# Optimization experiments

Measured on AMD Instinct MI355X. Metric: run time of the kernel, lower is better.

Reference implementation:

```python
import jax, jax.numpy as jnp
import numpy as np

# RBF_Conv2d config (matches init_kwargs)
KH = KW = 3
STRIDE = 1
OUT_CH = 256
IN_CH = 64
STD = 2.0  # gauss RBF std (activate_param[0])


def setup_inputs() -> dict:
    key = jax.random.key(0)
    k1, k2 = jax.random.split(key)
    x = jax.random.normal(k1, (16, IN_CH, 56, 56), dtype=jnp.float32)
    # kaiming_uniform_ on fan_in = IN_CH*KH*KW = 576 -> bound = sqrt(6/576)
    bound = float(np.sqrt(6.0 / (IN_CH * KH * KW)))
    weight = jax.random.uniform(k2, (OUT_CH, IN_CH * KH * KW), dtype=jnp.float32,
                                minval=-bound, maxval=bound)
    return {"x": x, "weight": weight}


def _cdist_conv(x, weight):
    # im2col: [B, C*KH*KW, Ho, Wo]; channel ordering (c, kh, kw) matches F.unfold
    patches = jax.lax.conv_general_dilated_patches(
        x, (KH, KW), (STRIDE, STRIDE), 'VALID')
    B, Kdim, Ho, Wo = patches.shape
    win = patches.reshape(B, Kdim, Ho * Wo).transpose(0, 2, 1)  # [B, P, K]
    # Euclidean distance via the expansion ||w||^2 + ||c||^2 - 2 w.c (no [B,P,K,O] tensor)
    w2 = jnp.sum(win * win, axis=-1, keepdims=True)            # [B, P, 1]
    c2 = jnp.sum(weight * weight, axis=-1)[None, None, :]      # [1, 1, O]
    d2 = w2 + c2 - 2.0 * jnp.einsum('bpk,ok->bpo', win, weight)
    dist = jnp.sqrt(jnp.maximum(d2, 1e-12))                    # [B, P, O]
    return dist, (B, Ho, Wo)


def reference(x, weight):
    dist, (B, Ho, Wo) = _cdist_conv(x, weight)
    # gauss RBF: exp(-d^2 / (2*std^2))
    act = jnp.exp(-(dist * dist) / (2.0 * STD * STD))
    # permute back to [B, O, Ho, Wo] like the torch code
    return act.transpose(0, 2, 1).reshape(B, OUT_CH, Ho, Wo)
```

## Files before the change

### kernel.cpp

```cpp
#include <hip/hip_runtime.h>
#include <hip/hip_bf16.h>
#include <stdint.h>

#define BATCH 16
#define IN_CH 64
#define HIN 56
#define WIN_ 56
#define HO 54
#define WO 54
#define P_PER_B (HO*WO)
#define P_PAD 2944
#define OUT_CH 256
#define KDIM 576
#define NPIX (HIN*WIN_)
#define XT_PIX 3264

typedef __attribute__((ext_vector_type(8))) short short8;
typedef __attribute__((ext_vector_type(4))) float f32x4;

__device__ __forceinline__ unsigned short f2bf(float f) {
    unsigned int u = __float_as_uint(f);
    unsigned int r = (u + 0x7fffu + ((u >> 16) & 1u)) >> 16;
    return (unsigned short)r;
}


__global__ void prep_weight(const float* __restrict__ w, short* __restrict__ wbf,
                            float* __restrict__ c2) {
    int o = blockIdx.x;
    int lane = threadIdx.x;
    float s = 0.f;
    #pragma unroll
    for (int j = 0; j < 9; ++j) {
        int k = j * 64 + lane;
        int c = k / 9, tap = k % 9;
        float v = w[o * KDIM + k];
        s += v * v;
        ((unsigned short*)wbf)[o * KDIM + tap * 64 + c] = f2bf(v);
    }
    #pragma unroll
    for (int off = 32; off > 0; off >>= 1) s += __shfl_down(s, off);
    if (lane == 0) c2[o] = s;
}

__global__ __launch_bounds__(256) void transpose_kernel(
    const float* __restrict__ x, short* __restrict__ xT, float* __restrict__ s) {
    __shared__ short lds[64 * 65];
    __shared__ float red[256];
    const int b    = blockIdx.x / 49;
    const int pix0 = (blockIdx.x % 49) * 64;
    const int tid  = threadIdx.x;
    const int quarter = tid >> 6;
    const int pix  = tid & 63;
    const float* xb = x + (size_t)b * IN_CH * NPIX + pix0 + pix;
    float acc = 0.f;
    #pragma unroll
    for (int it = 0; it < 16; ++it) {
        int c = quarter * 16 + it;
        float v = xb[c * NPIX];
        acc += v * v;
        lds[pix * 65 + c] = (short)f2bf(v);
    }
    red[tid] = acc;
    __syncthreads();
    const int cs = tid & 63;
    short* xTb = xT + ((size_t)b * XT_PIX + pix0) * 64;
    #pragma unroll
    for (int it = 0; it < 16; ++it) {
        int pixs = quarter * 16 + it;
        xTb[(size_t)pixs * 64 + cs] = lds[pixs * 65 + cs];
    }
    if (tid < 64)
        s[b * NPIX + pix0 + tid] = red[tid] + red[64 + tid] + red[128 + tid] + red[192 + tid];
}

__global__ void w2_kernel(const float* __restrict__ s, float* __restrict__ w2) {
    int t = blockIdx.x * 256 + threadIdx.x;
    if (t >= BATCH * P_PER_B) return;
    int b = t / P_PER_B, p = t % P_PER_B;
    int oh = p / WO, ow = p % WO;
    const float* sp = s + b * NPIX + oh * WIN_ + ow;
    float acc = 0.f;
    #pragma unroll
    for (int kh = 0; kh < 3; ++kh)
        #pragma unroll
        for (int kw = 0; kw < 3; ++kw)
            acc += sp[kh * WIN_ + kw];
    w2[b * P_PAD + p] = acc;
}


#define AS1(p) ((const __attribute__((address_space(1))) void*)(p))
#define AS3(p) ((__attribute__((address_space(3))) void*)(p))

__global__ __launch_bounds__(256) void gemm_rbf(
    const short* __restrict__ xT, const short* __restrict__ wbf,
    const float* __restrict__ w2, const float* __restrict__ c2,
    float* __restrict__ out) {
    __shared__ __align__(16) short lds_a[352 * 64];
    __shared__ __align__(16) short lds_b[2 * 128 * 64];

    const int mt = blockIdx.x;
    const int b  = mt / 23;
    const int p0 = (mt % 23) * 128;
    const int n0 = blockIdx.y * 128;

    const int tid  = threadIdx.x;
    const int wave = tid >> 6;
    const int lane = tid & 63;
    const int r16  = lane & 15;
    const int quad = lane >> 4;
    const int wm = (wave >> 1) * 64;
    const int wn = (wave & 1) * 64;

    const int oh_base  = p0 / WO;
    const int ihw_base = oh_base * WIN_;

    const int srow = lane >> 3;
    const int scx  = (lane & 7) ^ srow;

    const short* aSrc = xT + ((size_t)b * XT_PIX + ihw_base + srow) * 64 + scx * 8;
    #pragma unroll
    for (int i = 0; i < 11; ++i) {
        int rb8 = (wave * 11 + i) * 8;
        __builtin_amdgcn_global_load_lds(AS1(aSrc + (size_t)rb8 * 64),
                                         AS3(lds_a + rb8 * 64), 16, 0, 0);
    }
    const short* gbB[4];
    #pragma unroll
    for (int i = 0; i < 4; ++i) {
        int row = (wave * 4 + i) * 8 + srow;
        gbB[i] = wbf + (size_t)(n0 + row) * KDIM + scx * 8;
        __builtin_amdgcn_global_load_lds(AS1(gbB[i]),
                                         AS3(lds_b + (wave * 4 + i) * 512), 16, 0, 0);
    }

    int ihw_rel[4];
    #pragma unroll
    for (int ms = 0; ms < 4; ++ms) {
        int p = p0 + wm + ms * 16 + r16;
        if (p > P_PER_B - 1) p = P_PER_B - 1;
        int oh = p / WO, ow = p - oh * WO;
        ihw_rel[ms] = oh * WIN_ + ow - ihw_base;
    }
    const int xq = r16 & 7;

    f32x4 acc[4][4];
    #pragma unroll
    for (int i = 0; i < 4; ++i)
        #pragma unroll
        for (int j = 0; j < 4; ++j)
            acc[i][j] = (f32x4){0.f, 0.f, 0.f, 0.f};

    __syncthreads();

    constexpr int dtab_l[9] = {0, 1, 2, 56, 57, 58, 112, 113, 114};
    #pragma unroll
    for (int kt = 0; kt < 9; ++kt) {
        if (kt < 8) {
            short* dstB = lds_b + ((kt + 1) & 1) * (128 * 64);
            #pragma unroll
            for (int i = 0; i < 4; ++i)
                __builtin_amdgcn_global_load_lds(AS1(gbB[i] + (kt + 1) * 64),
                                                 AS3(dstB + (wave * 4 + i) * 512), 16, 0, 0);
        }
        const short* lb = lds_b + (kt & 1) * (128 * 64);
        const int dt = dtab_l[kt];
        __builtin_amdgcn_s_setprio(1);
        #pragma unroll
        for (int ks = 0; ks < 2; ++ks) {
            short8 af[4], bfr[4];
            #pragma unroll
            for (int ms = 0; ms < 4; ++ms) {
                int rl = ihw_rel[ms] + dt;
                af[ms] = *(const short8*)(lds_a + rl * 64
                                                + (((ks * 4 + quad) ^ (rl & 7)) * 8));
            }
            #pragma unroll
            for (int ns = 0; ns < 4; ++ns)
                bfr[ns] = *(const short8*)(lb + (wn + ns * 16 + r16) * 64
                                              + (((ks * 4 + quad) ^ xq) * 8));
            #pragma unroll
            for (int ms = 0; ms < 4; ++ms)
                #pragma unroll
                for (int ns = 0; ns < 4; ++ns)
                    acc[ms][ns] = __builtin_amdgcn_mfma_f32_16x16x32_bf16(
                        af[ms], bfr[ns], acc[ms][ns], 0, 0, 0);
        }
        __builtin_amdgcn_s_setprio(0);
        if (kt < 8) __syncthreads();
    }

    float* lf = (float*)lds_a;
    const int col  = tid & 31;
    const int rb   = tid >> 5;
    const int pcol = p0 + col * 4;
    const bool pok = (pcol < P_PER_B);
    f32x4 w2v = *(const f32x4*)(w2 + b * P_PAD + pcol);

    #pragma unroll
    for (int s = 0; s < 2; ++s) {
        __syncthreads();
        if ((wave & 1) == s) {
            #pragma unroll
            for (int ms = 0; ms < 4; ++ms) {
                int pl = wm + ms * 16 + quad * 4;
                #pragma unroll
                for (int ns = 0; ns < 4; ++ns) {
                    int od = ns * 16 + r16;
                    *(f32x4*)(lf + od * 132 + pl) = acc[ms][ns];
                }
            }
        }
        __syncthreads();
        #pragma unroll
        for (int pass = 0; pass < 8; ++pass) {
            int row = pass * 8 + rb;
            int o   = n0 + s * 64 + row;
            f32x4 a = *(const f32x4*)(lf + row * 132 + col * 4);
            float c2o = c2[o];
            f32x4 v;
            #pragma unroll
            for (int r = 0; r < 4; ++r) {
                float d2 = w2v[r] + c2o - 2.0f * a[r];
                d2 = fmaxf(d2, 1e-12f);
                v[r] = __expf(-0.125f * d2);
            }
            if (pok)
                *(f32x4*)(out + ((size_t)(b * OUT_CH + o)) * P_PER_B + pcol) = v;
        }
    }
}


extern "C" void kernel_launch(void* const* d_in, const int* in_sizes, int n_in,
                              void* d_out, int out_size, void* d_ws, size_t ws_size,
                              hipStream_t stream) {
    const float* x = (const float*)d_in[0];
    const float* w = (const float*)d_in[1];
    float* out = (float*)d_out;

    char* ws = (char*)d_ws;
    const size_t wbf_bytes = (size_t)OUT_CH * KDIM * 2;
    const size_t c2_bytes  = 1024;
    const size_t w2_bytes  = (size_t)BATCH * P_PAD * 4;
    const size_t s_bytes   = (size_t)BATCH * NPIX * 4;
    short* wbf = (short*)ws;
    float* c2  = (float*)(ws + wbf_bytes);
    float* w2  = (float*)(ws + wbf_bytes + c2_bytes);
    float* s   = (float*)(ws + wbf_bytes + c2_bytes + w2_bytes);
    short* xT  = (short*)(ws + wbf_bytes + c2_bytes + w2_bytes + s_bytes);

    hipLaunchKernelGGL(prep_weight, dim3(OUT_CH), dim3(64), 0, stream, w, wbf, c2);
    hipLaunchKernelGGL(transpose_kernel, dim3(16 * 49), dim3(256), 0, stream, x, xT, s);
    hipLaunchKernelGGL(w2_kernel, dim3((BATCH * P_PER_B + 255) / 256), dim3(256), 0, stream, s, w2);
    hipLaunchKernelGGL(gemm_rbf, dim3(23 * BATCH, OUT_CH / 128), dim3(256), 0, stream,
                       xT, wbf, w2, c2, out);
}
```

Measured before the change: 107.7 us.

## Halve N tile, load weights directly into registers, drop LDS B buffer and syncs

Shrinks each block's output-channel tile from 128 to 64 and doubles the grid in that dimension. Weight fragments now go straight from global memory into double-buffered registers instead of being staged in LDS, which removes the per-k-step barriers and the LDS B buffer. With less LDS and fewer accumulators per thread, two blocks per CU can be resident (launch bounds 256,2). In exchange, the input patch tile in LDS is reloaded twice as many times across the grid, and weight reads become per-lane global loads that lean on cache.

```diff
diff --git a/kernel.cpp b/kernel.cpp
--- a/kernel.cpp
+++ b/kernel.cpp
@@ -93,17 +93,16 @@
 #define AS1(p) ((const __attribute__((address_space(1))) void*)(p))
 #define AS3(p) ((__attribute__((address_space(3))) void*)(p))
 
-__global__ __launch_bounds__(256) void gemm_rbf(
+__global__ __launch_bounds__(256, 2) void gemm_rbf(
     const short* __restrict__ xT, const short* __restrict__ wbf,
     const float* __restrict__ w2, const float* __restrict__ c2,
     float* __restrict__ out) {
     __shared__ __align__(16) short lds_a[352 * 64];
-    __shared__ __align__(16) short lds_b[2 * 128 * 64];
 
     const int mt = blockIdx.x;
     const int b  = mt / 23;
     const int p0 = (mt % 23) * 128;
-    const int n0 = blockIdx.y * 128;
+    const int n0 = blockIdx.y * 64;
 
     const int tid  = threadIdx.x;
     const int wave = tid >> 6;
@@ -111,7 +110,7 @@
     const int r16  = lane & 15;
     const int quad = lane >> 4;
     const int wm = (wave >> 1) * 64;
-    const int wn = (wave & 1) * 64;
+    const int wn = (wave & 1) * 32;
 
     const int oh_base  = p0 / WO;
     const int ihw_base = oh_base * WIN_;
@@ -125,14 +124,6 @@
         int rb8 = (wave * 11 + i) * 8;
         __builtin_amdgcn_global_load_lds(AS1(aSrc + (size_t)rb8 * 64),
                                          AS3(lds_a + rb8 * 64), 16, 0, 0);
-    }
-    const short* gbB[4];
-    #pragma unroll
-    for (int i = 0; i < 4; ++i) {
-        int row = (wave * 4 + i) * 8 + srow;
-        gbB[i] = wbf + (size_t)(n0 + row) * KDIM + scx * 8;
-        __builtin_amdgcn_global_load_lds(AS1(gbB[i]),
-                                         AS3(lds_b + (wave * 4 + i) * 512), 16, 0, 0);
     }
 
     int ihw_rel[4];
@@ -143,14 +134,25 @@
         int oh = p / WO, ow = p - oh * WO;
         ihw_rel[ms] = oh * WIN_ + ow - ihw_base;
     }
-    const int xq = r16 & 7;
-
-    f32x4 acc[4][4];
+
+    const short* wp[2];
+    #pragma unroll
+    for (int ns = 0; ns < 2; ++ns)
+        wp[ns] = wbf + (size_t)(n0 + wn + ns * 16 + r16) * KDIM + quad * 8;
+
+    f32x4 acc[4][2];
     #pragma unroll
     for (int i = 0; i < 4; ++i)
         #pragma unroll
-        for (int j = 0; j < 4; ++j)
+        for (int j = 0; j < 2; ++j)
             acc[i][j] = (f32x4){0.f, 0.f, 0.f, 0.f};
+
+    short8 breg[2][2][2];
+    #pragma unroll
+    for (int ns = 0; ns < 2; ++ns)
+        #pragma unroll
+        for (int ks = 0; ks < 2; ++ks)
+            breg[0][ns][ks] = *(const short8*)(wp[ns] + ks * 32);
 
     __syncthreads();
 
@@ -158,18 +160,17 @@
     #pragma unroll
     for (int kt = 0; kt < 9; ++kt) {
         if (kt < 8) {
-            short* dstB = lds_b + ((kt + 1) & 1) * (128 * 64);
             #pragma unroll
-            for (int i = 0; i < 4; ++i)
-                __builtin_amdgcn_global_load_lds(AS1(gbB[i] + (kt + 1) * 64),
-                                                 AS3(dstB + (wave * 4 + i) * 512), 16, 0, 0);
-        }
-        const short* lb = lds_b + (kt & 1) * (128 * 64);
+            for (int ns = 0; ns < 2; ++ns)
+                #pragma unroll
+                for (int ks = 0; ks < 2; ++ks)
+                    breg[(kt + 1) & 1][ns][ks] =
+                        *(const short8*)(wp[ns] + (kt + 1) * 64 + ks * 32);
+        }
         const int dt = dtab_l[kt];
-        __builtin_amdgcn_s_setprio(1);
         #pragma unroll
         for (int ks = 0; ks < 2; ++ks) {
-            short8 af[4], bfr[4];
+            short8 af[4];
             #pragma unroll
             for (int ms = 0; ms < 4; ++ms) {
                 int rl = ihw_rel[ms] + dt;
@@ -177,18 +178,12 @@
                                                 + (((ks * 4 + quad) ^ (rl & 7)) * 8));
             }
             #pragma unroll
-            for (int ns = 0; ns < 4; ++ns)
-                bfr[ns] = *(const short8*)(lb + (wn + ns * 16 + r16) * 64
-                                              + (((ks * 4 + quad) ^ xq) * 8));
-            #pragma unroll
             for (int ms = 0; ms < 4; ++ms)
                 #pragma unroll
-                for (int ns = 0; ns < 4; ++ns)
+                for (int ns = 0; ns < 2; ++ns)
                     acc[ms][ns] = __builtin_amdgcn_mfma_f32_16x16x32_bf16(
-                        af[ms], bfr[ns], acc[ms][ns], 0, 0, 0);
-        }
-        __builtin_amdgcn_s_setprio(0);
-        if (kt < 8) __syncthreads();
+                        af[ms], breg[kt & 1][ns][ks], acc[ms][ns], 0, 0, 0);
+        }
     }
 
     float* lf = (float*)lds_a;
@@ -198,37 +193,32 @@
     const bool pok = (pcol < P_PER_B);
     f32x4 w2v = *(const f32x4*)(w2 + b * P_PAD + pcol);
 
-    #pragma unroll
-    for (int s = 0; s < 2; ++s) {
-        __syncthreads();
-        if ((wave & 1) == s) {
-            #pragma unroll
-            for (int ms = 0; ms < 4; ++ms) {
-                int pl = wm + ms * 16 + quad * 4;
-                #pragma unroll
-                for (int ns = 0; ns < 4; ++ns) {
-                    int od = ns * 16 + r16;
-                    *(f32x4*)(lf + od * 132 + pl) = acc[ms][ns];
-                }
-            }
-        }
-        __syncthreads();
-        #pragma unroll
-        for (int pass = 0; pass < 8; ++pass) {
-            int row = pass * 8 + rb;
-            int o   = n0 + s * 64 + row;
-            f32x4 a = *(const f32x4*)(lf + row * 132 + col * 4);
-            float c2o = c2[o];
-            f32x4 v;
-            #pragma unroll
-            for (int r = 0; r < 4; ++r) {
-                float d2 = w2v[r] + c2o - 2.0f * a[r];
-                d2 = fmaxf(d2, 1e-12f);
-                v[r] = __expf(-0.125f * d2);
-            }
-            if (pok)
-                *(f32x4*)(out + ((size_t)(b * OUT_CH + o)) * P_PER_B + pcol) = v;
-        }
+    __syncthreads();
+    #pragma unroll
+    for (int ms = 0; ms < 4; ++ms) {
+        int pl = wm + ms * 16 + quad * 4;
+        #pragma unroll
+        for (int ns = 0; ns < 2; ++ns) {
+            int od = wn + ns * 16 + r16;
+            *(f32x4*)(lf + od * 132 + pl) = acc[ms][ns];
+        }
+    }
+    __syncthreads();
+    #pragma unroll
+    for (int pass = 0; pass < 8; ++pass) {
+        int row = pass * 8 + rb;
+        int o   = n0 + row;
+        f32x4 a = *(const f32x4*)(lf + row * 132 + col * 4);
+        float c2o = c2[o];
+        f32x4 v;
+        #pragma unroll
+        for (int r = 0; r < 4; ++r) {
+            float d2 = w2v[r] + c2o - 2.0f * a[r];
+            d2 = fmaxf(d2, 1e-12f);
+            v[r] = __expf(-0.125f * d2);
+        }
+        if (pok)
+            *(f32x4*)(out + ((size_t)(b * OUT_CH + o)) * P_PER_B + pcol) = v;
     }
 }
 
@@ -254,6 +244,6 @@
     hipLaunchKernelGGL(prep_weight, dim3(OUT_CH), dim3(64), 0, stream, w, wbf, c2);
     hipLaunchKernelGGL(transpose_kernel, dim3(16 * 49), dim3(256), 0, stream, x, xT, s);
     hipLaunchKernelGGL(w2_kernel, dim3((BATCH * P_PER_B + 255) / 256), dim3(256), 0, stream, s, w2);
-    hipLaunchKernelGGL(gemm_rbf, dim3(23 * BATCH, OUT_CH / 128), dim3(256), 0, stream,
+    hipLaunchKernelGGL(gemm_rbf, dim3(23 * BATCH, 4), dim3(256), 0, stream,
                        xT, wbf, w2, c2, out);
 }
```

Result: slower. 112.2 us (+4.2%).
